# Kernel optimization log

Measured on AMD Instinct MI355X. Metric: run time of the kernel, lower is better.

The kernel has to match this reference:

```python
import jax, jax.numpy as jnp
import numpy as np

B, T, D = 2, 1024, 2048      # batch, seq_len, hidden_size
H, DK = 8, 128               # num_heads, head_k_dim
DV = 2 * DK                  # head_v_dim = head_dim * expand_v
KD, VD = H * DK, H * DV      # key_dim, value_dim
KCONV = 4                    # short conv kernel size
EPS = 1e-5


def _short_conv(x, w):
    # depthwise causal conv1d + SiLU; x: [B,T,C], w: [C,K]
    Klen = w.shape[1]
    xp = jnp.pad(x, ((0, 0), (Klen - 1, 0), (0, 0)))
    win = jnp.stack([xp[:, j:j + x.shape[1], :] for j in range(Klen)], axis=-1)  # [B,T,C,K]
    return jax.nn.silu(jnp.einsum('btck,ck->btc', win, w))


def _l2norm(x):
    return x * jax.lax.rsqrt(jnp.sum(x * x, -1, keepdims=True) + 1e-6)


def reference(hidden_states, q_w, k_w, v_w, a_w, b_w, g_w, o_w,
              q_conv_w, k_conv_w, v_conv_w, A_log, dt_bias, o_norm_w):
    h = hidden_states
    # projections + short depthwise causal conv + SiLU
    q = _short_conv(h @ q_w.T, q_conv_w)        # [B,T,KD]
    k = _short_conv(h @ k_w.T, k_conv_w)        # [B,T,KD]
    v = _short_conv(h @ v_w.T, v_conv_w)        # [B,T,VD]
    q = _l2norm(q.reshape(B, T, H, DK))
    k = _l2norm(k.reshape(B, T, H, DK))
    v = v.reshape(B, T, H, DV)
    beta = jax.nn.sigmoid(h @ b_w.T)                                 # [B,T,H]
    g = -jnp.exp(A_log) * jax.nn.softplus(h @ a_w.T + dt_bias)       # [B,T,H] decay log-gate
    scale = DK ** -0.5

    def step(S, xs):
        # S: [B,H,DK,DV] recurrent state; gated delta rule update
        qt, kt, vt, gt, bt = xs
        S = S * jnp.exp(gt)[..., None, None]
        kv = jnp.einsum('bhk,bhkv->bhv', kt, S)
        u = (vt - kv) * bt[..., None]
        S = S + jnp.einsum('bhk,bhv->bhkv', kt, u)
        ot = jnp.einsum('bhk,bhkv->bhv', qt, S) * scale
        return S, ot

    xs = (q.transpose(1, 0, 2, 3), k.transpose(1, 0, 2, 3), v.transpose(1, 0, 2, 3),
          g.transpose(1, 0, 2), beta.transpose(1, 0, 2))
    S0 = jnp.zeros((B, H, DK, DV), q.dtype)
    _, o = jax.lax.scan(step, S0, xs)
    o = o.transpose(1, 0, 2, 3)                       # [B,T,H,DV]
    # gated RMSNorm (FusedRMSNormGated) + output projection
    gate = (h @ g_w.T).reshape(B, T, H, DV)
    o = o * jax.lax.rsqrt(jnp.mean(o * o, -1, keepdims=True) + EPS) * o_norm_w
    o = o * jax.nn.silu(gate)
    return o.reshape(B, T, VD) @ o_w.T


def setup_inputs() -> dict:
    key = jax.random.key(0)
    ks = jax.random.split(key, 14)
    n = lambda i, shp, sc: jax.random.normal(ks[i], shp, jnp.float32) * sc
    return {
        'hidden_states': n(0, (B, T, D), 1.0),
        'q_w': n(1, (KD, D), 0.02), 'k_w': n(2, (KD, D), 0.02), 'v_w': n(3, (VD, D), 0.02),
        'a_w': n(4, (H, D), 0.02), 'b_w': n(5, (H, D), 0.02),
        'g_w': n(6, (VD, D), 0.02), 'o_w': n(7, (D, VD), 0.02),
        'q_conv_w': n(8, (KD, KCONV), 0.3), 'k_conv_w': n(9, (KD, KCONV), 0.3),
        'v_conv_w': n(10, (VD, KCONV), 0.3),
        'A_log': jnp.log(jax.random.uniform(ks[11], (H,), jnp.float32, 0.5, 16.0)),
        'dt_bias': n(12, (H,), 1.0),
        'o_norm_w': jnp.ones((DV,), jnp.float32),
    }
```

## Files before the change

kernel.cpp:

```cpp
#include <hip/hip_runtime.h>
#include <cstdint>

#define T_LEN 1024
#define NBIG  6400
#define SCALE_Q 0.08838834764831843f

typedef __bf16 bf16;
typedef __bf16 bf16x8 __attribute__((ext_vector_type(8)));
typedef float  f32x4  __attribute__((ext_vector_type(4)));

__device__ __forceinline__ unsigned short f2bf(float f) {
  unsigned int u = __builtin_bit_cast(unsigned int, f);
  u += 0x7FFFu + ((u >> 16) & 1u);
  return (unsigned short)(u >> 16);
}
__device__ __forceinline__ float bf2f(unsigned short u) {
  return __builtin_bit_cast(float, (unsigned int)u << 16);
}
__device__ __forceinline__ float silu_f(float x) { return x / (1.f + __expf(-x)); }

#define GLDS(src, dst) \
  __builtin_amdgcn_global_load_lds( \
      (__attribute__((address_space(1))) void*)(void*)(src), \
      (__attribute__((address_space(3))) void*)(void*)(dst), 16, 0, 0)

__global__ __launch_bounds__(256) void cvt_bf16(const float* __restrict__ in,
                                                unsigned short* __restrict__ out, int n4) {
  int idx = blockIdx.x * 256 + threadIdx.x;
  if (idx >= n4) return;
  float4 f = ((const float4*)in)[idx];
  ushort4 o = { f2bf(f.x), f2bf(f.y), f2bf(f.z), f2bf(f.w) };
  ((ushort4*)out)[idx] = o;
}

__global__ __launch_bounds__(256) void build_w(
    const float* __restrict__ qw, const float* __restrict__ kw,
    const float* __restrict__ vw, const float* __restrict__ gw,
    const float* __restrict__ aw, const float* __restrict__ bw,
    unsigned short* __restrict__ W) {
  int idx = blockIdx.x * 256 + threadIdx.x;
  int r = idx >> 9;
  int c = (idx & 511) << 2;
  const float* src;
  if      (r < 1024) src = qw + (size_t)r * 2048;
  else if (r < 2048) src = kw + (size_t)(r - 1024) * 2048;
  else if (r < 4096) src = vw + (size_t)(r - 2048) * 2048;
  else if (r < 6144) src = gw + (size_t)(r - 4096) * 2048;
  else if (r < 6152) src = aw + (size_t)(r - 6144) * 2048;
  else if (r < 6160) src = bw + (size_t)(r - 6152) * 2048;
  else               src = nullptr;
  ushort4 o;
  if (src) {
    float4 f = *(const float4*)(src + c);
    o = { f2bf(f.x), f2bf(f.y), f2bf(f.z), f2bf(f.w) };
  } else {
    o = { 0, 0, 0, 0 };
  }
  *(ushort4*)(W + (size_t)r * 2048 + c) = o;
}

template <int BN, int WN, int T, bool BF16OUT>
__global__ __launch_bounds__(T, 4) void gemm_pipe(
    const bf16* __restrict__ A, const bf16* __restrict__ Bm,
    void* __restrict__ Cv, int N, int K) {
  constexpr int AI = (128 * 32) / (T * 8);
  constexpr int BI = (BN * 32) / (T * 8);
  constexpr int LOADS = AI + BI;
  __shared__ bf16 LA[3][128 * 32];
  __shared__ bf16 LB[3][BN * 32];
  const int tid = threadIdx.x;
  const int lane = tid & 63;
  const int wid = tid >> 6;
  const int wm = wid / WN, wn = wid % WN;
  const int bid = blockIdx.x;
  const int xcd = bid & 7, jj = bid >> 3;
  const long brow = (long)(xcd + 8 * (jj & 1)) * 128;
  const long bcol = (long)(jj >> 1) * BN;

  f32x4 acc[4][4];
#pragma unroll
  for (int m = 0; m < 4; ++m)
#pragma unroll
    for (int n = 0; n < 4; ++n)
#pragma unroll
      for (int r = 0; r < 4; ++r) acc[m][n][r] = 0.f;

  const bf16* AgS[AI];
  const bf16* BgS[BI];
  int adst[AI], bdst[BI];
#pragma unroll
  for (int e = 0; e < AI; ++e) {
    const int flat = e * T + tid;
    const int row = flat >> 2;
    const int sl = (flat & 3) ^ ((row >> 1) & 3);
    AgS[e] = A + (brow + row) * (long)K + sl * 8;
    adst[e] = flat * 8;
  }
#pragma unroll
  for (int e = 0; e < BI; ++e) {
    const int flat = e * T + tid;
    const int row = flat >> 2;
    const int sl = (flat & 3) ^ ((row >> 1) & 3);
    BgS[e] = Bm + (bcol + row) * (long)K + sl * 8;
    bdst[e] = flat * 8;
  }

#define STAGE(kt, sb)                                              \
  {                                                                \
    const long ko = (long)(kt) * 32;                               \
    _Pragma("unroll")                                              \
    for (int e = 0; e < AI; ++e) GLDS(AgS[e] + ko, &LA[sb][0] + adst[e]); \
    _Pragma("unroll")                                              \
    for (int e = 0; e < BI; ++e) GLDS(BgS[e] + ko, &LB[sb][0] + bdst[e]); \
  }
#define WAIT_VM()                                                  \
  if constexpr (LOADS == 3) asm volatile("s_waitcnt vmcnt(3)" ::: "memory"); \
  else                      asm volatile("s_waitcnt vmcnt(4)" ::: "memory");

  const int r16 = lane & 15;
  const int ks = lane >> 4;
  const int pso = (ks ^ ((r16 >> 1) & 3)) * 8;
  int rdA[4], rdB[4];
#pragma unroll
  for (int i = 0; i < 4; ++i) rdA[i] = (wm * 64 + i * 16 + r16) * 32 + pso;
#pragma unroll
  for (int j = 0; j < 4; ++j) rdB[j] = (wn * 64 + j * 16 + r16) * 32 + pso;

  const int nkt = K >> 5;
  STAGE(0, 0);
  STAGE(1, 1);
  WAIT_VM();
  __builtin_amdgcn_s_barrier();

  bf16x8 af[4], bfr[4];
#pragma unroll
  for (int i = 0; i < 4; ++i) af[i] = *(const bf16x8*)(&LA[0][0] + rdA[i]);
#pragma unroll
  for (int j = 0; j < 4; ++j) bfr[j] = *(const bf16x8*)(&LB[0][0] + rdB[j]);

  for (int kt = 0; kt < nkt; ++kt) {
    const int kts = (kt + 2 < nkt) ? kt + 2 : nkt - 1;
    const int sb = (kt + 2) % 3;
    const int nb = (kt + 1) % 3;

    STAGE(kts, sb);
    __builtin_amdgcn_s_setprio(1);
#pragma unroll
    for (int i = 0; i < 4; ++i)
#pragma unroll
      for (int j = 0; j < 4; ++j)
        acc[i][j] = __builtin_amdgcn_mfma_f32_16x16x32_bf16(af[i], bfr[j], acc[i][j], 0, 0, 0);
    __builtin_amdgcn_s_setprio(0);

    asm volatile("s_waitcnt lgkmcnt(0)" ::: "memory");
    WAIT_VM();
    __builtin_amdgcn_s_barrier();
#pragma unroll
    for (int i = 0; i < 4; ++i) af[i] = *(const bf16x8*)(&LA[nb][0] + rdA[i]);
#pragma unroll
    for (int j = 0; j < 4; ++j) bfr[j] = *(const bf16x8*)(&LB[nb][0] + rdB[j]);
  }
#undef STAGE
#undef WAIT_VM

  const long row0 = brow + wm * 64 + ((lane >> 4) * 4);
  const long col0 = bcol + wn * 64 + (lane & 15);
#pragma unroll
  for (int m = 0; m < 4; ++m)
#pragma unroll
    for (int n = 0; n < 4; ++n)
#pragma unroll
      for (int r = 0; r < 4; ++r) {
        if constexpr (BF16OUT)
          ((unsigned short*)Cv)[(row0 + m * 16 + r) * (long)N + col0 + n * 16] = f2bf(acc[m][n][r]);
        else
          ((float*)Cv)[(row0 + m * 16 + r) * (long)N + col0 + n * 16] = acc[m][n][r];
      }
}

template <int M, int N, int K, bool TOGLOB, int NW>
__device__ __forceinline__ void mm_nt_lds(const unsigned short* A, const unsigned short* B,
                                          float* outF, unsigned short* outG, int ldg, int tid) {
  constexpr int NT16 = N / 16;
  constexpr int PW = (M / 16) * NT16 / NW;
  const int w = tid >> 6, l = tid & 63;
  const int row = l & 15, ko = (l >> 4) * 8;
  f32x4 acc[PW];
#pragma unroll
  for (int i = 0; i < PW; ++i)
#pragma unroll
    for (int r = 0; r < 4; ++r) acc[i][r] = 0.f;
#pragma unroll
  for (int i = 0; i < PW; ++i) {
    const int ti = w + NW * i;
    const int rt = ti / NT16, ct = ti % NT16;
#pragma unroll
    for (int kk = 0; kk < K / 32; ++kk) {
      bf16x8 af = *(const bf16x8*)(A + (rt * 16 + row) * K + kk * 32 + ko);
      bf16x8 bf = *(const bf16x8*)(B + (ct * 16 + row) * K + kk * 32 + ko);
      acc[i] = __builtin_amdgcn_mfma_f32_16x16x32_bf16(af, bf, acc[i], 0, 0, 0);
    }
  }
#pragma unroll
  for (int i = 0; i < PW; ++i) {
    const int ti = w + NW * i;
    const int rt = ti / NT16, ct = ti % NT16;
    const int r0 = rt * 16 + (l >> 4) * 4;
    const int col = ct * 16 + (l & 15);
#pragma unroll
    for (int r = 0; r < 4; ++r) {
      if constexpr (TOGLOB) outG[(size_t)(r0 + r) * ldg + col] = f2bf(acc[i][r]);
      else                  outF[(r0 + r) * N + col] = acc[i][r];
    }
  }
}

template <int K>
__device__ __forceinline__ void mm64_acc(const unsigned short* A, const unsigned short* B,
                                         f32x4 acc[2], int w, int row, int ko) {
#pragma unroll
  for (int i = 0; i < 2; ++i) {
    const int ti = w + 8 * i;
    const int rt = ti >> 2, ct = ti & 3;
#pragma unroll
    for (int kk = 0; kk < K / 32; ++kk) {
      bf16x8 af = *(const bf16x8*)(A + (rt * 16 + row) * K + kk * 32 + ko);
      bf16x8 bf = *(const bf16x8*)(B + (ct * 16 + row) * K + kk * 32 + ko);
      acc[i] = __builtin_amdgcn_mfma_f32_16x16x32_bf16(af, bf, acc[i], 0, 0, 0);
    }
  }
}

__global__ __launch_bounds__(512, 1) void chunk_prep(
    const unsigned short* __restrict__ Y,
    const float* __restrict__ qcw, const float* __restrict__ kcw, const float* __restrict__ vcw,
    const float* __restrict__ A_log, const float* __restrict__ dt_bias,
    unsigned short* __restrict__ Wg, unsigned short* __restrict__ Ubg,
    unsigned short* __restrict__ Attg, unsigned short* __restrict__ Qgg,
    unsigned short* __restrict__ KgTg, float* __restrict__ decg) {
  __shared__ unsigned short Kb_s[64 * 128];
  __shared__ unsigned short Qb_s[64 * 128];
  __shared__ unsigned short VbT_s[256 * 64];
  __shared__ unsigned short Mb_s[4096];
  __shared__ unsigned short Xrow_s[2][4096];
  __shared__ unsigned short Xt_s[2][4096];
  __shared__ unsigned short Yt_s[4096];
  __shared__ float F1_s[4096];
  __shared__ float carr_s[64];
  __shared__ float beta_s[64];

  const int tid = threadIdx.x;
  const int w = tid >> 6, l = tid & 63;
  const int row16 = l & 15, ko = (l >> 4) * 8;
  const int ch = blockIdx.x;
  const int bh = ch >> 4, p = ch & 15;
  const int b = bh >> 3, h = bh & 7;
  const size_t tbase = (size_t)b * T_LEN + p * 64;
  const bool head = (p == 0);

  if (tid < 64) {
    const unsigned short* Yr = Y + (tbase + tid) * NBIG;
    float a = bf2f(Yr[6144 + h]) + dt_bias[h];
    float sp = (a > 20.f) ? a : log1pf(expf(a));
    float g = -expf(A_log[h]) * sp;
    float bp = bf2f(Yr[6152 + h]);
    beta_s[tid] = 1.f / (1.f + expf(-bp));
    float c = g;
#pragma unroll
    for (int d = 1; d < 64; d <<= 1) {
      float y = __shfl_up(c, d);
      if (tid >= d) c += y;
    }
    carr_s[tid] = c;
    if (tid == 63) decg[ch] = __expf(c);
  }
  __syncthreads();

  {
    const bool isQ = (tid < 256);
    const int wk = tid & 255;
    const int quad = wk & 31, tg = wk >> 5;
    const int c = quad * 4;
    const float* cw = isQ ? qcw : kcw;
    const int cb = (isQ ? 0 : 1024) + h * 128 + c;
    float4 wv[4];
#pragma unroll
    for (int e = 0; e < 4; ++e) wv[e] = ((const float4*)cw)[h * 128 + c + e];
    float rows[11][4];
#pragma unroll
    for (int r = 0; r < 11; ++r) {
      if (head && tg == 0 && r < 3) {
        rows[r][0] = rows[r][1] = rows[r][2] = rows[r][3] = 0.f;
      } else {
        const ushort4 x = *(const ushort4*)(Y + (tbase + tg * 8 - 3 + r) * NBIG + cb);
        rows[r][0] = bf2f(x.x); rows[r][1] = bf2f(x.y);
        rows[r][2] = bf2f(x.z); rows[r][3] = bf2f(x.w);
      }
    }
    unsigned short* dst = isQ ? Qb_s : Kb_s;
    const float sc = isQ ? SCALE_Q : 1.f;
#pragma unroll
    for (int i = 0; i < 8; ++i) {
      float acc[4], ss = 0.f;
#pragma unroll
      for (int e = 0; e < 4; ++e) {
        float a = wv[e].x * rows[i][e];
        a = fmaf(wv[e].y, rows[i + 1][e], a);
        a = fmaf(wv[e].z, rows[i + 2][e], a);
        a = fmaf(wv[e].w, rows[i + 3][e], a);
        a = silu_f(a);
        acc[e] = a;
        ss += a * a;
      }
#pragma unroll
      for (int m = 16; m >= 1; m >>= 1) ss += __shfl_xor(ss, m);
      const float rn = rsqrtf(ss + 1e-6f) * sc;
      ushort4 o = {f2bf(acc[0] * rn), f2bf(acc[1] * rn), f2bf(acc[2] * rn), f2bf(acc[3] * rn)};
      *(ushort4*)(dst + (tg * 8 + i) * 128 + c) = o;
    }
  }
  {
    const int quad = tid & 63, tg = tid >> 6;
    const int c = quad * 4;
    float4 wv[4];
#pragma unroll
    for (int e = 0; e < 4; ++e) wv[e] = ((const float4*)vcw)[h * 256 + c + e];
    float rows[11][4];
#pragma unroll
    for (int r = 0; r < 11; ++r) {
      if (head && tg == 0 && r < 3) {
        rows[r][0] = rows[r][1] = rows[r][2] = rows[r][3] = 0.f;
      } else {
        const ushort4 x = *(const ushort4*)(Y + (tbase + tg * 8 - 3 + r) * NBIG + 2048 + h * 256 + c);
        rows[r][0] = bf2f(x.x); rows[r][1] = bf2f(x.y);
        rows[r][2] = bf2f(x.z); rows[r][3] = bf2f(x.w);
      }
    }
#pragma unroll
    for (int i = 0; i < 8; ++i) {
      const int t = tg * 8 + i;
      const float bt = beta_s[t];
#pragma unroll
      for (int e = 0; e < 4; ++e) {
        float a = wv[e].x * rows[i][e];
        a = fmaf(wv[e].y, rows[i + 1][e], a);
        a = fmaf(wv[e].z, rows[i + 2][e], a);
        a = fmaf(wv[e].w, rows[i + 3][e], a);
        VbT_s[(c + e) * 64 + t] = f2bf(bt * silu_f(a));
      }
    }
  }
  __syncthreads();

  {
    f32x4 acc[2];
#pragma unroll
    for (int i = 0; i < 2; ++i)
#pragma unroll
      for (int r = 0; r < 4; ++r) acc[i][r] = 0.f;
    mm64_acc<128>(Kb_s, Kb_s, acc, w, row16, ko);
#pragma unroll
    for (int i = 0; i < 2; ++i) {
      const int ti = w + 8 * i;
      const int rt = ti >> 2, ct = ti & 3;
      const int r0 = rt * 16 + (l >> 4) * 4;
      const int col = ct * 16 + (l & 15);
#pragma unroll
      for (int r = 0; r < 4; ++r) {
        const int t = r0 + r, j = col;
        const float av = (j < t) ? beta_s[t] * __expf(carr_s[t] - carr_s[j]) * acc[i][r] : 0.f;
        const float dg = (t == j) ? 1.f : 0.f;
        Mb_s[t * 64 + j] = f2bf(dg + av);
        const float x0 = dg - av;
        F1_s[t * 64 + j] = x0;
        const unsigned short xb = f2bf(x0);
        Xrow_s[0][t * 64 + j] = xb;
        Xt_s[0][j * 64 + t] = xb;
      }
    }
  }
  __syncthreads();
  int cur = 0;
  for (int it = 0; it < 5; ++it) {
    {
      f32x4 acc[2];
#pragma unroll
      for (int i = 0; i < 2; ++i)
#pragma unroll
        for (int r = 0; r < 4; ++r) acc[i][r] = 0.f;
      mm64_acc<64>(Mb_s, Xt_s[cur], acc, w, row16, ko);
#pragma unroll
      for (int i = 0; i < 2; ++i) {
        const int ti = w + 8 * i;
        const int rt = ti >> 2, ct = ti & 3;
        const int r0 = rt * 16 + (l >> 4) * 4;
        const int col = ct * 16 + (l & 15);
#pragma unroll
        for (int r = 0; r < 4; ++r)
          Yt_s[col * 64 + (r0 + r)] = f2bf(acc[i][r]);
      }
    }
    __syncthreads();
    {
      f32x4 acc[2];
#pragma unroll
      for (int i = 0; i < 2; ++i)
#pragma unroll
        for (int r = 0; r < 4; ++r) acc[i][r] = 0.f;
      mm64_acc<64>(Xrow_s[cur], Yt_s, acc, w, row16, ko);
#pragma unroll
      for (int i = 0; i < 2; ++i) {
        const int ti = w + 8 * i;
        const int rt = ti >> 2, ct = ti & 3;
        const int r0 = rt * 16 + (l >> 4) * 4;
        const int col = ct * 16 + (l & 15);
#pragma unroll
        for (int r = 0; r < 4; ++r) {
          const int idx = (r0 + r) * 64 + col;
          const float xn = 2.f * F1_s[idx] - acc[i][r];
          F1_s[idx] = xn;
          const unsigned short xb = f2bf(xn);
          Xrow_s[cur ^ 1][idx] = xb;
          Xt_s[cur ^ 1][col * 64 + (r0 + r)] = xb;
        }
      }
    }
    cur ^= 1;
    __syncthreads();
  }
  const unsigned short* Xfin = Xrow_s[cur];
  const float ctot = carr_s[63];
  {
    f32x4 acc[2];
#pragma unroll
    for (int i = 0; i < 2; ++i)
#pragma unroll
      for (int r = 0; r < 4; ++r) acc[i][r] = 0.f;
    mm64_acc<128>(Qb_s, Kb_s, acc, w, row16, ko);
#pragma unroll
    for (int i = 0; i < 2; ++i) {
      const int ti = w + 8 * i;
      const int rt = ti >> 2, ct = ti & 3;
      const int r0 = rt * 16 + (l >> 4) * 4;
      const int col = ct * 16 + (l & 15);
#pragma unroll
      for (int r = 0; r < 4; ++r) {
        const int t = r0 + r, j = col;
        const float av = (j <= t) ? __expf(carr_s[t] - carr_s[j]) * acc[i][r] : 0.f;
        Attg[(size_t)ch * 4096 + t * 64 + j] = f2bf(av);
      }
    }
  }
#pragma unroll
  for (int i = 0; i < 16; ++i) {
    const int idx = i * 512 + tid;
    const int t = idx >> 7;
    Qgg[(size_t)ch * 8192 + idx] = f2bf(__expf(carr_s[t]) * bf2f(Qb_s[idx]));
  }
#pragma unroll
  for (int i = 0; i < 16; ++i) {
    const int idx = i * 512 + tid;
    const int d = idx >> 6, t = idx & 63;
    KgTg[(size_t)ch * 8192 + idx] = f2bf(__expf(ctot - carr_s[t]) * bf2f(Kb_s[t * 128 + d]));
  }
  __syncthreads();
  unsigned short* KbgT = Qb_s;
#pragma unroll
  for (int i = 0; i < 16; ++i) {
    const int idx = i * 512 + tid;
    const int d = idx >> 6, t = idx & 63;
    KbgT[idx] = f2bf(beta_s[t] * __expf(carr_s[t]) * bf2f(Kb_s[t * 128 + d]));
  }
  __syncthreads();
  mm_nt_lds<64, 128, 64, true, 8>(Xfin, KbgT, nullptr, Wg + (size_t)ch * 8192, 128, tid);
  mm_nt_lds<64, 256, 64, true, 8>(Xfin, VbT_s, nullptr, Ubg + (size_t)ch * 16384, 256, tid);
}

__device__ __forceinline__ void p2_stage(
    const unsigned short* Wg, const unsigned short* Attg, const unsigned short* Qgg,
    const unsigned short* KgTg, const unsigned short* Ubg,
    int ch, int vb, unsigned short* buf, int tid) {
#pragma unroll
  for (int i = 0; i < 2; ++i) {
    const int f = i * 512 + tid;
    GLDS(Wg + (size_t)ch * 8192 + f * 8, (char*)buf + f * 16);
  }
  {
    const int f = tid;
    GLDS(Attg + (size_t)ch * 4096 + f * 8, (char*)(buf + 8192) + f * 16);
  }
#pragma unroll
  for (int i = 0; i < 2; ++i) {
    const int f = i * 512 + tid;
    GLDS(Qgg + (size_t)ch * 8192 + f * 8, (char*)(buf + 12288) + f * 16);
  }
#pragma unroll
  for (int i = 0; i < 2; ++i) {
    const int f = i * 512 + tid;
    GLDS(KgTg + (size_t)ch * 8192 + f * 8, (char*)(buf + 20480) + f * 16);
  }
  if (tid < 256) {
    const int f = tid;
    const int t = f >> 2, c8 = f & 3;
    GLDS(Ubg + (size_t)ch * 16384 + t * 256 + vb * 32 + c8 * 8, (char*)(buf + 28672) + f * 16);
  }
}

__global__ __launch_bounds__(512, 1) void scan_chunks(
    const unsigned short* __restrict__ Wg, const unsigned short* __restrict__ Ubg,
    const unsigned short* __restrict__ Attg, const unsigned short* __restrict__ Qgg,
    const unsigned short* __restrict__ KgTg, const float* __restrict__ decg,
    float* __restrict__ osc) {
  __shared__ float StT_s[32 * 128];
  __shared__ unsigned short StTb_s[32 * 128];
  __shared__ unsigned short uT_s[32 * 64];
  __shared__ unsigned short stage_s[2][30720];

  const int tid = threadIdx.x;
  const int w = tid >> 6, l = tid & 63;
  const int row = l & 15, ko = (l >> 4) * 8;
  const int blk = blockIdx.x;
  const int vb = blk >> 4, bh = blk & 15;
  const int b = bh >> 3, h = bh & 7;

  for (int i = tid; i < 4096; i += 512) { StT_s[i] = 0.f; StTb_s[i] = 0; }
  p2_stage(Wg, Attg, Qgg, KgTg, Ubg, bh * 16, vb, stage_s[0], tid);

  for (int p = 0; p < 16; ++p) {
    unsigned short* bufc = stage_s[p & 1];
    const unsigned short* Wl   = bufc;
    const unsigned short* Attl = bufc + 8192;
    const unsigned short* Qgl  = bufc + 12288;
    const unsigned short* KgTl = bufc + 20480;
    const unsigned short* Ubl  = bufc + 28672;
    __syncthreads();

    f32x4 uacc;
#pragma unroll
    for (int r = 0; r < 4; ++r) uacc[r] = 0.f;
    const int rt = w >> 1, ct = w & 1;
#pragma unroll
    for (int kk = 0; kk < 4; ++kk) {
      bf16x8 af = *(const bf16x8*)(Wl + (rt * 16 + row) * 128 + kk * 32 + ko);
      bf16x8 bf = *(const bf16x8*)(StTb_s + (ct * 16 + row) * 128 + kk * 32 + ko);
      uacc = __builtin_amdgcn_mfma_f32_16x16x32_bf16(af, bf, uacc, 0, 0, 0);
    }
    {
      const int r0 = rt * 16 + (l >> 4) * 4;
      const int col = ct * 16 + (l & 15);
#pragma unroll
      for (int r = 0; r < 4; ++r) {
        const int t = r0 + r;
        const float ubv = bf2f(Ubl[t * 32 + col]);
        uT_s[col * 64 + t] = f2bf(ubv - uacc[r]);
      }
    }
    __syncthreads();
    if (p < 15)
      p2_stage(Wg, Attg, Qgg, KgTg, Ubg, bh * 16 + p + 1, vb, stage_s[(p + 1) & 1], tid);

    f32x4 oacc;
#pragma unroll
    for (int r = 0; r < 4; ++r) oacc[r] = 0.f;
#pragma unroll
    for (int kk = 0; kk < 4; ++kk) {
      bf16x8 af = *(const bf16x8*)(Qgl + (rt * 16 + row) * 128 + kk * 32 + ko);
      bf16x8 bf = *(const bf16x8*)(StTb_s + (ct * 16 + row) * 128 + kk * 32 + ko);
      oacc = __builtin_amdgcn_mfma_f32_16x16x32_bf16(af, bf, oacc, 0, 0, 0);
    }
#pragma unroll
    for (int kk = 0; kk < 2; ++kk) {
      bf16x8 af = *(const bf16x8*)(Attl + (rt * 16 + row) * 64 + kk * 32 + ko);
      bf16x8 bf = *(const bf16x8*)(uT_s + (ct * 16 + row) * 64 + kk * 32 + ko);
      oacc = __builtin_amdgcn_mfma_f32_16x16x32_bf16(af, bf, oacc, 0, 0, 0);
    }
    f32x4 sacc[2];
#pragma unroll
    for (int i = 0; i < 2; ++i)
#pragma unroll
      for (int r = 0; r < 4; ++r) sacc[i][r] = 0.f;
#pragma unroll
    for (int i = 0; i < 2; ++i) {
      const int ti = w + 8 * i;
      const int srt = ti >> 3, sct = ti & 7;
#pragma unroll
      for (int kk = 0; kk < 2; ++kk) {
        bf16x8 af = *(const bf16x8*)(uT_s + (srt * 16 + row) * 64 + kk * 32 + ko);
        bf16x8 bf = *(const bf16x8*)(KgTl + (sct * 16 + row) * 64 + kk * 32 + ko);
        sacc[i] = __builtin_amdgcn_mfma_f32_16x16x32_bf16(af, bf, sacc[i], 0, 0, 0);
      }
    }
    const float dec = decg[bh * 16 + p];
    __syncthreads();

    {
      const int r0 = rt * 16 + (l >> 4) * 4;
      const int col = ct * 16 + (l & 15);
#pragma unroll
      for (int r = 0; r < 4; ++r) {
        const size_t trow = (size_t)b * T_LEN + p * 64 + r0 + r;
        osc[(trow * 8 + h) * 256 + vb * 32 + col] = oacc[r];
      }
    }
#pragma unroll
    for (int i = 0; i < 2; ++i) {
      const int ti = w + 8 * i;
      const int srt = ti >> 3, sct = ti & 7;
      const int r0 = srt * 16 + (l >> 4) * 4;
      const int cold = sct * 16 + (l & 15);
#pragma unroll
      for (int r = 0; r < 4; ++r) {
        const int idx = (r0 + r) * 128 + cold;
        const float sn = fmaf(dec, StT_s[idx], sacc[i][r]);
        StT_s[idx] = sn;
        StTb_s[idx] = f2bf(sn);
      }
    }
  }
}

__global__ __launch_bounds__(256) void rmsgate(
    const float* __restrict__ ob, const unsigned short* __restrict__ Y,
    const float* __restrict__ onw, unsigned short* __restrict__ Obf) {
  const int bt = blockIdx.x;
  const int tid = threadIdx.x;
  const int c = tid * 8;
  const float* orow = ob + (size_t)bt * 2048 + c;
  const unsigned short* grow = Y + (size_t)bt * NBIG + 4096 + c;
  const float4 o0 = *(const float4*)orow, o1 = *(const float4*)(orow + 4);
  const ushort4 g0 = *(const ushort4*)grow, g1 = *(const ushort4*)(grow + 4);
  const float ov[8] = {o0.x, o0.y, o0.z, o0.w, o1.x, o1.y, o1.z, o1.w};
  const float gv[8] = {bf2f(g0.x), bf2f(g0.y), bf2f(g0.z), bf2f(g0.w),
                       bf2f(g1.x), bf2f(g1.y), bf2f(g1.z), bf2f(g1.w)};
  float ss = 0.f;
#pragma unroll
  for (int e = 0; e < 8; ++e) ss += ov[e] * ov[e];
#pragma unroll
  for (int m = 16; m >= 1; m >>= 1) ss += __shfl_xor(ss, m);
  const float rn = rsqrtf(ss * (1.f / 256.f) + 1e-5f);
  const int dv = c & 255;
  unsigned short rr[8];
#pragma unroll
  for (int e = 0; e < 8; ++e) {
    const float val = ov[e] * rn * onw[dv + e] * silu_f(gv[e]);
    rr[e] = f2bf(val);
  }
  ushort4 r0 = {rr[0], rr[1], rr[2], rr[3]};
  ushort4 r1 = {rr[4], rr[5], rr[6], rr[7]};
  *(ushort4*)(Obf + (size_t)bt * 2048 + c) = r0;
  *(ushort4*)(Obf + (size_t)bt * 2048 + c + 4) = r1;
}

extern "C" void kernel_launch(void* const* d_in, const int* in_sizes, int n_in,
                              void* d_out, int out_size, void* d_ws, size_t ws_size,
                              hipStream_t stream) {
  (void)in_sizes; (void)n_in; (void)out_size; (void)ws_size;
  const float* h    = (const float*)d_in[0];
  const float* qw   = (const float*)d_in[1];
  const float* kw   = (const float*)d_in[2];
  const float* vw   = (const float*)d_in[3];
  const float* aw   = (const float*)d_in[4];
  const float* bw   = (const float*)d_in[5];
  const float* gw   = (const float*)d_in[6];
  const float* ow   = (const float*)d_in[7];
  const float* qcw  = (const float*)d_in[8];
  const float* kcw  = (const float*)d_in[9];
  const float* vcw  = (const float*)d_in[10];
  const float* Alog = (const float*)d_in[11];
  const float* dtb  = (const float*)d_in[12];
  const float* onw  = (const float*)d_in[13];

  char* ws = (char*)d_ws;
  size_t off = 0;
  auto alloc = [&](size_t bytes) {
    char* p = ws + off;
    off = (off + bytes + 255) & ~(size_t)255;
    return p;
  };
  unsigned short* hbf  = (unsigned short*)alloc(2048ull * 2048 * 2);
  unsigned short* Wb   = (unsigned short*)alloc((size_t)NBIG * 2048 * 2);
  unsigned short* owb  = (unsigned short*)alloc(2048ull * 2048 * 2);
  unsigned short* Ybf  = (unsigned short*)alloc(2048ull * NBIG * 2);
  float* osc           = (float*)alloc(2048ull * 2048 * 4);
  unsigned short* Obf  = (unsigned short*)alloc(2048ull * 2048 * 2);
  unsigned short* Wg   = (unsigned short*)alloc(256ull * 8192 * 2);
  unsigned short* Ubg  = (unsigned short*)alloc(256ull * 16384 * 2);
  unsigned short* Attg = (unsigned short*)alloc(256ull * 4096 * 2);
  unsigned short* Qgg  = (unsigned short*)alloc(256ull * 8192 * 2);
  unsigned short* KgTg = (unsigned short*)alloc(256ull * 8192 * 2);
  float* decg          = (float*)alloc(256ull * 4);

  cvt_bf16<<<4096, 256, 0, stream>>>(h, hbf, 1048576);
  build_w<<<12800, 256, 0, stream>>>(qw, kw, vw, gw, aw, bw, Wb);
  cvt_bf16<<<4096, 256, 0, stream>>>(ow, owb, 1048576);
  gemm_pipe<256, 4, 512, true><<<400, 512, 0, stream>>>(
      (const bf16*)hbf, (const bf16*)Wb, Ybf, NBIG, 2048);
  chunk_prep<<<256, 512, 0, stream>>>(Ybf, qcw, kcw, vcw, Alog, dtb,
                                      Wg, Ubg, Attg, Qgg, KgTg, decg);
  scan_chunks<<<128, 512, 0, stream>>>(Wg, Ubg, Attg, Qgg, KgTg, decg, osc);
  rmsgate<<<2048, 256, 0, stream>>>(osc, Ybf, onw, Obf);
  gemm_pipe<128, 2, 256, false><<<256, 256, 0, stream>>>(
      (const bf16*)Obf, (const bf16*)owb, d_out, 2048, 2048);
}
```

Before: 225.5 us.

## Split output GEMM along K with atomics and halve scan value-block width

```diff
diff --git a/kernel.cpp b/kernel.cpp
--- a/kernel.cpp
+++ b/kernel.cpp
@@ -31,6 +31,13 @@
   float4 f = ((const float4*)in)[idx];
   ushort4 o = { f2bf(f.x), f2bf(f.y), f2bf(f.z), f2bf(f.w) };
   ((ushort4*)out)[idx] = o;
+}
+
+__global__ __launch_bounds__(256) void zero_f32(float* __restrict__ p, int n4) {
+  int idx = blockIdx.x * 256 + threadIdx.x;
+  if (idx >= n4) return;
+  float4 z = {0.f, 0.f, 0.f, 0.f};
+  ((float4*)p)[idx] = z;
 }
 
 __global__ __launch_bounds__(256) void build_w(
@@ -59,10 +66,10 @@
   *(ushort4*)(W + (size_t)r * 2048 + c) = o;
 }
 
-template <int BN, int WN, int T, bool BF16OUT>
+template <int BN, int WN, int T, bool BF16OUT, bool ATOMIC>
 __global__ __launch_bounds__(T, 4) void gemm_pipe(
     const bf16* __restrict__ A, const bf16* __restrict__ Bm,
-    void* __restrict__ Cv, int N, int K) {
+    void* __restrict__ Cv, int N, int K, int ldk) {
   constexpr int AI = (128 * 32) / (T * 8);
   constexpr int BI = (BN * 32) / (T * 8);
   constexpr int LOADS = AI + BI;
@@ -72,7 +79,9 @@
   const int lane = tid & 63;
   const int wid = tid >> 6;
   const int wm = wid / WN, wn = wid % WN;
-  const int bid = blockIdx.x;
+  const int bidAll = blockIdx.x;
+  const int bid = ATOMIC ? (bidAll & 255) : bidAll;
+  const long kofs = ATOMIC ? (long)(bidAll >> 8) * K : 0;
   const int xcd = bid & 7, jj = bid >> 3;
   const long brow = (long)(xcd + 8 * (jj & 1)) * 128;
   const long bcol = (long)(jj >> 1) * BN;
@@ -93,7 +102,7 @@
     const int flat = e * T + tid;
     const int row = flat >> 2;
     const int sl = (flat & 3) ^ ((row >> 1) & 3);
-    AgS[e] = A + (brow + row) * (long)K + sl * 8;
+    AgS[e] = A + (brow + row) * (long)ldk + kofs + sl * 8;
     adst[e] = flat * 8;
   }
 #pragma unroll
@@ -101,7 +110,7 @@
     const int flat = e * T + tid;
     const int row = flat >> 2;
     const int sl = (flat & 3) ^ ((row >> 1) & 3);
-    BgS[e] = Bm + (bcol + row) * (long)K + sl * 8;
+    BgS[e] = Bm + (bcol + row) * (long)ldk + kofs + sl * 8;
     bdst[e] = flat * 8;
   }
 
@@ -171,16 +180,19 @@
     for (int n = 0; n < 4; ++n)
 #pragma unroll
       for (int r = 0; r < 4; ++r) {
-        if constexpr (BF16OUT)
-          ((unsigned short*)Cv)[(row0 + m * 16 + r) * (long)N + col0 + n * 16] = f2bf(acc[m][n][r]);
+        const long idx = (row0 + m * 16 + r) * (long)N + col0 + n * 16;
+        if constexpr (ATOMIC)
+          atomicAdd((float*)Cv + idx, acc[m][n][r]);
+        else if constexpr (BF16OUT)
+          ((unsigned short*)Cv)[idx] = f2bf(acc[m][n][r]);
         else
-          ((float*)Cv)[(row0 + m * 16 + r) * (long)N + col0 + n * 16] = acc[m][n][r];
-      }
-}
-
-template <int M, int N, int K, bool TOGLOB, int NW>
+          ((float*)Cv)[idx] = acc[m][n][r];
+      }
+}
+
+template <int M, int N, int K, int NW>
 __device__ __forceinline__ void mm_nt_lds(const unsigned short* A, const unsigned short* B,
-                                          float* outF, unsigned short* outG, int ldg, int tid) {
+                                          unsigned short* outG, int ldg, int tid) {
   constexpr int NT16 = N / 16;
   constexpr int PW = (M / 16) * NT16 / NW;
   const int w = tid >> 6, l = tid & 63;
@@ -208,10 +220,8 @@
     const int r0 = rt * 16 + (l >> 4) * 4;
     const int col = ct * 16 + (l & 15);
 #pragma unroll
-    for (int r = 0; r < 4; ++r) {
-      if constexpr (TOGLOB) outG[(size_t)(r0 + r) * ldg + col] = f2bf(acc[i][r]);
-      else                  outF[(r0 + r) * N + col] = acc[i][r];
-    }
+    for (int r = 0; r < 4; ++r)
+      outG[(size_t)(r0 + r) * ldg + col] = f2bf(acc[i][r]);
   }
 }
 
@@ -245,7 +255,6 @@
   __shared__ unsigned short Xrow_s[2][4096];
   __shared__ unsigned short Xt_s[2][4096];
   __shared__ unsigned short Yt_s[4096];
-  __shared__ float F1_s[4096];
   __shared__ float carr_s[64];
   __shared__ float beta_s[64];
 
@@ -352,6 +361,7 @@
   }
   __syncthreads();
 
+  float xf[2][4];
   {
     f32x4 acc[2];
 #pragma unroll
@@ -372,7 +382,7 @@
         const float dg = (t == j) ? 1.f : 0.f;
         Mb_s[t * 64 + j] = f2bf(dg + av);
         const float x0 = dg - av;
-        F1_s[t * 64 + j] = x0;
+        xf[i][r] = x0;
         const unsigned short xb = f2bf(x0);
         Xrow_s[0][t * 64 + j] = xb;
         Xt_s[0][j * 64 + t] = xb;
@@ -416,11 +426,10 @@
         const int col = ct * 16 + (l & 15);
 #pragma unroll
         for (int r = 0; r < 4; ++r) {
-          const int idx = (r0 + r) * 64 + col;
-          const float xn = 2.f * F1_s[idx] - acc[i][r];
-          F1_s[idx] = xn;
+          const float xn = 2.f * xf[i][r] - acc[i][r];
+          xf[i][r] = xn;
           const unsigned short xb = f2bf(xn);
-          Xrow_s[cur ^ 1][idx] = xb;
+          Xrow_s[cur ^ 1][(r0 + r) * 64 + col] = xb;
           Xt_s[cur ^ 1][col * 64 + (r0 + r)] = xb;
         }
       }
@@ -472,8 +481,8 @@
     KbgT[idx] = f2bf(beta_s[t] * __expf(carr_s[t]) * bf2f(Kb_s[t * 128 + d]));
   }
   __syncthreads();
-  mm_nt_lds<64, 128, 64, true, 8>(Xfin, KbgT, nullptr, Wg + (size_t)ch * 8192, 128, tid);
-  mm_nt_lds<64, 256, 64, true, 8>(Xfin, VbT_s, nullptr, Ubg + (size_t)ch * 16384, 256, tid);
+  mm_nt_lds<64, 128, 64, 8>(Xfin, KbgT, Wg + (size_t)ch * 8192, 128, tid);
+  mm_nt_lds<64, 256, 64, 8>(Xfin, VbT_s, Ubg + (size_t)ch * 16384, 256, tid);
 }
 
 __device__ __forceinline__ void p2_stage(
@@ -499,10 +508,10 @@
     const int f = i * 512 + tid;
     GLDS(KgTg + (size_t)ch * 8192 + f * 8, (char*)(buf + 20480) + f * 16);
   }
-  if (tid < 256) {
+  if (tid < 128) {
     const int f = tid;
-    const int t = f >> 2, c8 = f & 3;
-    GLDS(Ubg + (size_t)ch * 16384 + t * 256 + vb * 32 + c8 * 8, (char*)(buf + 28672) + f * 16);
+    const int t = f >> 1, c8 = f & 1;
+    GLDS(Ubg + (size_t)ch * 16384 + t * 256 + vb * 16 + c8 * 8, (char*)(buf + 28672) + f * 16);
   }
 }
 
@@ -511,10 +520,10 @@
     const unsigned short* __restrict__ Attg, const unsigned short* __restrict__ Qgg,
     const unsigned short* __restrict__ KgTg, const float* __restrict__ decg,
     float* __restrict__ osc) {
-  __shared__ float StT_s[32 * 128];
-  __shared__ unsigned short StTb_s[32 * 128];
-  __shared__ unsigned short uT_s[32 * 64];
-  __shared__ unsigned short stage_s[2][30720];
+  __shared__ float StT_s[16 * 128];
+  __shared__ unsigned short StTb_s[16 * 128];
+  __shared__ unsigned short uT_s[16 * 64];
+  __shared__ unsigned short stage_s[2][29696];
 
   const int tid = threadIdx.x;
   const int w = tid >> 6, l = tid & 63;
@@ -522,8 +531,9 @@
   const int blk = blockIdx.x;
   const int vb = blk >> 4, bh = blk & 15;
   const int b = bh >> 3, h = bh & 7;
-
-  for (int i = tid; i < 4096; i += 512) { StT_s[i] = 0.f; StTb_s[i] = 0; }
+  const bool uw = (w < 4);
+
+  for (int i = tid; i < 2048; i += 512) { StT_s[i] = 0.f; StTb_s[i] = 0; }
   p2_stage(Wg, Attg, Qgg, KgTg, Ubg, bh * 16, vb, stage_s[0], tid);
 
   for (int p = 0; p < 16; ++p) {
@@ -538,20 +548,19 @@
     f32x4 uacc;
 #pragma unroll
     for (int r = 0; r < 4; ++r) uacc[r] = 0.f;
-    const int rt = w >> 1, ct = w & 1;
-#pragma unroll
-    for (int kk = 0; kk < 4; ++kk) {
-      bf16x8 af = *(const bf16x8*)(Wl + (rt * 16 + row) * 128 + kk * 32 + ko);
-      bf16x8 bf = *(const bf16x8*)(StTb_s + (ct * 16 + row) * 128 + kk * 32 + ko);
-      uacc = __builtin_amdgcn_mfma_f32_16x16x32_bf16(af, bf, uacc, 0, 0, 0);
-    }
-    {
-      const int r0 = rt * 16 + (l >> 4) * 4;
-      const int col = ct * 16 + (l & 15);
+    if (uw) {
+#pragma unroll
+      for (int kk = 0; kk < 4; ++kk) {
+        bf16x8 af = *(const bf16x8*)(Wl + (w * 16 + row) * 128 + kk * 32 + ko);
+        bf16x8 bf = *(const bf16x8*)(StTb_s + row * 128 + kk * 32 + ko);
+        uacc = __builtin_amdgcn_mfma_f32_16x16x32_bf16(af, bf, uacc, 0, 0, 0);
+      }
+      const int r0 = w * 16 + (l >> 4) * 4;
+      const int col = l & 15;
 #pragma unroll
       for (int r = 0; r < 4; ++r) {
         const int t = r0 + r;
-        const float ubv = bf2f(Ubl[t * 32 + col]);
+        const float ubv = bf2f(Ubl[t * 16 + col]);
         uT_s[col * 64 + t] = f2bf(ubv - uacc[r]);
       }
     }
@@ -562,56 +571,47 @@
     f32x4 oacc;
 #pragma unroll
     for (int r = 0; r < 4; ++r) oacc[r] = 0.f;
-#pragma unroll
-    for (int kk = 0; kk < 4; ++kk) {
-      bf16x8 af = *(const bf16x8*)(Qgl + (rt * 16 + row) * 128 + kk * 32 + ko);
-      bf16x8 bf = *(const bf16x8*)(StTb_s + (ct * 16 + row) * 128 + kk * 32 + ko);
-      oacc = __builtin_amdgcn_mfma_f32_16x16x32_bf16(af, bf, oacc, 0, 0, 0);
-    }
+    if (uw) {
+#pragma unroll
+      for (int kk = 0; kk < 4; ++kk) {
+        bf16x8 af = *(const bf16x8*)(Qgl + (w * 16 + row) * 128 + kk * 32 + ko);
+        bf16x8 bf = *(const bf16x8*)(StTb_s + row * 128 + kk * 32 + ko);
+        oacc = __builtin_amdgcn_mfma_f32_16x16x32_bf16(af, bf, oacc, 0, 0, 0);
+      }
+#pragma unroll
+      for (int kk = 0; kk < 2; ++kk) {
+        bf16x8 af = *(const bf16x8*)(Attl + (w * 16 + row) * 64 + kk * 32 + ko);
+        bf16x8 bf = *(const bf16x8*)(uT_s + row * 64 + kk * 32 + ko);
+        oacc = __builtin_amdgcn_mfma_f32_16x16x32_bf16(af, bf, oacc, 0, 0, 0);
+      }
+    }
+    f32x4 sacc;
+#pragma unroll
+    for (int r = 0; r < 4; ++r) sacc[r] = 0.f;
 #pragma unroll
     for (int kk = 0; kk < 2; ++kk) {
-      bf16x8 af = *(const bf16x8*)(Attl + (rt * 16 + row) * 64 + kk * 32 + ko);
-      bf16x8 bf = *(const bf16x8*)(uT_s + (ct * 16 + row) * 64 + kk * 32 + ko);
-      oacc = __builtin_amdgcn_mfma_f32_16x16x32_bf16(af, bf, oacc, 0, 0, 0);
-    }
-    f32x4 sacc[2];
-#pragma unroll
-    for (int i = 0; i < 2; ++i)
-#pragma unroll
-      for (int r = 0; r < 4; ++r) sacc[i][r] = 0.f;
-#pragma unroll
-    for (int i = 0; i < 2; ++i) {
-      const int ti = w + 8 * i;
-      const int srt = ti >> 3, sct = ti & 7;
-#pragma unroll
-      for (int kk = 0; kk < 2; ++kk) {
-        bf16x8 af = *(const bf16x8*)(uT_s + (srt * 16 + row) * 64 + kk * 32 + ko);
-        bf16x8 bf = *(const bf16x8*)(KgTl + (sct * 16 + row) * 64 + kk * 32 + ko);
-        sacc[i] = __builtin_amdgcn_mfma_f32_16x16x32_bf16(af, bf, sacc[i], 0, 0, 0);
-      }
+      bf16x8 af = *(const bf16x8*)(uT_s + row * 64 + kk * 32 + ko);
+      bf16x8 bf = *(const bf16x8*)(KgTl + (w * 16 + row) * 64 + kk * 32 + ko);
+      sacc = __builtin_amdgcn_mfma_f32_16x16x32_bf16(af, bf, sacc, 0, 0, 0);
     }
     const float dec = decg[bh * 16 + p];
     __syncthreads();
 
-    {
-      const int r0 = rt * 16 + (l >> 4) * 4;
-      const int col = ct * 16 + (l & 15);
+    if (uw) {
+      const int r0 = w * 16 + (l >> 4) * 4;
+      const int col = l & 15;
 #pragma unroll
       for (int r = 0; r < 4; ++r) {
         const size_t trow = (size_t)b * T_LEN + p * 64 + r0 + r;
-        osc[(trow * 8 + h) * 256 + vb * 32 + col] = oacc[r];
-      }
-    }
-#pragma unroll
-    for (int i = 0; i < 2; ++i) {
-      const int ti = w + 8 * i;
-      const int srt = ti >> 3, sct = ti & 7;
-      const int r0 = srt * 16 + (l >> 4) * 4;
-      const int cold = sct * 16 + (l & 15);
+        osc[(trow * 8 + h) * 256 + vb * 16 + col] = oacc[r];
+      }
+    }
+    {
+      const int cold = w * 16 + (l & 15);
 #pragma unroll
       for (int r = 0; r < 4; ++r) {
-        const int idx = (r0 + r) * 128 + cold;
-        const float sn = fmaf(dec, StT_s[idx], sacc[i][r]);
+        const int idx = ((l >> 4) * 4 + r) * 128 + cold;
+        const float sn = fmaf(dec, StT_s[idx], sacc[r]);
         StT_s[idx] = sn;
         StTb_s[idx] = f2bf(sn);
       }
@@ -693,12 +693,13 @@
   cvt_bf16<<<4096, 256, 0, stream>>>(h, hbf, 1048576);
   build_w<<<12800, 256, 0, stream>>>(qw, kw, vw, gw, aw, bw, Wb);
   cvt_bf16<<<4096, 256, 0, stream>>>(ow, owb, 1048576);
-  gemm_pipe<256, 4, 512, true><<<400, 512, 0, stream>>>(
-      (const bf16*)hbf, (const bf16*)Wb, Ybf, NBIG, 2048);
+  zero_f32<<<4096, 256, 0, stream>>>((float*)d_out, 1048576);
+  gemm_pipe<256, 4, 512, true, false><<<400, 512, 0, stream>>>(
+      (const bf16*)hbf, (const bf16*)Wb, Ybf, NBIG, 2048, 2048);
   chunk_prep<<<256, 512, 0, stream>>>(Ybf, qcw, kcw, vcw, Alog, dtb,
                                       Wg, Ubg, Attg, Qgg, KgTg, decg);
-  scan_chunks<<<128, 512, 0, stream>>>(Wg, Ubg, Attg, Qgg, KgTg, decg, osc);
+  scan_chunks<<<256, 512, 0, stream>>>(Wg, Ubg, Attg, Qgg, KgTg, decg, osc);
   rmsgate<<<2048, 256, 0, stream>>>(osc, Ybf, onw, Obf);
-  gemm_pipe<128, 2, 256, false><<<256, 256, 0, stream>>>(
-      (const bf16*)Obf, (const bf16*)owb, d_out, 2048, 2048);
-}
+  gemm_pipe<128, 2, 256, false, true><<<512, 256, 0, stream>>>(
+      (const bf16*)Obf, (const bf16*)owb, d_out, 2048, 1024, 2048);
+}
```

Measured after the change: 220.9 us. 1.02x faster.
